# Performance work log

Measured on AMD Instinct MI355X. Metric: run time of the kernel, lower is better.

Reference implementation:

```python
import jax, jax.numpy as jnp
import numpy as np

L_SEQ = 32768
H_FEAT = 512
P_STATE = 256  # state_size // 2 (conj_sym)
LOG_DT_MIN, LOG_DT_MAX = np.log(1e-3), np.log(1e-1)


def setup_inputs() -> dict:
    key = jax.random.key(0)
    ks = jax.random.split(key, 7)
    input_sequence = jax.random.normal(ks[0], (L_SEQ, H_FEAT), dtype=jnp.float32)
    # eigenvalue real parts must be negative for stability (HiPPO-LegS-like)
    lambda_real = -jax.random.uniform(ks[1], (P_STATE,), minval=0.1, maxval=1.0, dtype=jnp.float32)
    lambda_imag = jax.random.normal(ks[2], (P_STATE,), dtype=jnp.float32) * float(np.pi)
    b = jax.random.normal(ks[3], (P_STATE, H_FEAT, 2), dtype=jnp.float32) / np.sqrt(H_FEAT)
    c = jax.random.normal(ks[4], (H_FEAT, P_STATE, 2), dtype=jnp.float32) / np.sqrt(P_STATE)
    d = jax.random.normal(ks[5], (H_FEAT,), dtype=jnp.float32)
    # log-timestep init in [log(1e-3), log(1e-1)] as in init_log_steps
    delta = (LOG_DT_MIN + jax.random.uniform(ks[6], (P_STATE, 1), dtype=jnp.float32)
             * (LOG_DT_MAX - LOG_DT_MIN))
    return {"input_sequence": input_sequence, "lambda_real": lambda_real,
            "lambda_imag": lambda_imag, "b": b, "c": c, "d": d, "delta": delta}


def _binop(e_i, e_j):
    A_i, b_i = e_i
    A_j, b_j = e_j
    return A_j * A_i, A_j * b_i + b_j


def reference(input_sequence, lambda_real, lambda_imag, b, c, d, delta):
    # assemble complex parameters (stored as real [..., 2])
    Lam = lambda_real + 1j * lambda_imag            # [P]
    B = b[..., 0] + 1j * b[..., 1]                  # [P, H]
    C = c[..., 0] + 1j * c[..., 1]                  # [H, P]
    step = jnp.exp(delta[:, 0])                     # step_rescale = 1.0
    # bilinear discretization
    BL = 1.0 / (1.0 - (step / 2.0) * Lam)
    Lam_bar = BL * (1.0 + (step / 2.0) * Lam)       # [P]
    B_bar = (BL * step)[:, None] * B                # [P, H]
    # input projection: Bu[l] = B_bar @ u[l]
    Bu = jnp.einsum('lh,ph->lp', input_sequence.astype(Lam_bar.dtype), B_bar)  # [L, P]
    L = input_sequence.shape[0]
    Lam_el = jnp.broadcast_to(Lam_bar, (L, Lam_bar.shape[0]))
    _, xs = jax.lax.associative_scan(_binop, (Lam_el, Bu))  # xs: [L, P] complex states
    # output projection (conj_sym => factor 2, real part)
    ys = 2.0 * jnp.einsum('lp,hp->lh', xs, C).real  # [L, H]
    return ys + d * input_sequence
```

## Files before the change

### kernel.cpp

```cpp
#include <hip/hip_runtime.h>
#include <cstddef>

#define L_SEQ 32768
#define H_FEAT 512
#define P_STATE 256
#define N2 512
#define CS 32
#define NCH (L_SEQ / CS)

typedef __bf16 bf16x8 __attribute__((ext_vector_type(8)));
typedef float f32x4 __attribute__((ext_vector_type(4)));

#define GLDS16(g, l) __builtin_amdgcn_global_load_lds( \
    (const __attribute__((address_space(1))) void*)(g), \
    (__attribute__((address_space(3))) void*)(l), 16, 0, 0)

__device__ __forceinline__ unsigned bf_rne(float x) {
    unsigned u = __float_as_uint(x);
    return (u + 0x7fffu + ((u >> 16) & 1u)) >> 16;
}
__device__ __forceinline__ float bf_f(unsigned bits) {
    return __uint_as_float(bits << 16);
}

__global__ __launch_bounds__(256) void param_kernel(
    const float* __restrict__ lr, const float* __restrict__ li,
    const float* __restrict__ b,  const float* __restrict__ c,
    const float* __restrict__ delta,
    ushort* __restrict__ W_hi, ushort* __restrict__ W_lo,
    ushort* __restrict__ C2_hi, ushort* __restrict__ C2_lo,
    float2* __restrict__ Abar)
{
    int tid = blockIdx.x * blockDim.x + threadIdx.x;

    {
        int p = tid >> 9;
        int h = tid & 511;
        float step = expf(delta[p]);
        float zr = 0.5f * step * lr[p];
        float zi = 0.5f * step * li[p];
        float dr = 1.0f - zr, di = -zi;
        float den = dr * dr + di * di;
        float blr = dr / den, bli = -di / den;
        float bbr = blr * step, bbi = bli * step;
        float b0 = b[((size_t)(p * H_FEAT + h)) * 2 + 0];
        float b1 = b[((size_t)(p * H_FEAT + h)) * 2 + 1];
        float vr = bbr * b0 - bbi * b1;
        float vi = bbr * b1 + bbi * b0;
        unsigned hr = bf_rne(vr), hl = bf_rne(vr - bf_f(hr));
        unsigned ir = bf_rne(vi), il = bf_rne(vi - bf_f(ir));
        size_t o0 = (size_t)(2 * p) * H_FEAT + h;
        size_t o1 = (size_t)(2 * p + 1) * H_FEAT + h;
        W_hi[o0] = (ushort)hr; W_lo[o0] = (ushort)hl;
        W_hi[o1] = (ushort)ir; W_lo[o1] = (ushort)il;
    }

    {
        int h2 = tid >> 8;
        int p2 = tid & 255;
        float c0 =  2.0f * c[((size_t)(h2 * P_STATE + p2)) * 2 + 0];
        float c1 = -2.0f * c[((size_t)(h2 * P_STATE + p2)) * 2 + 1];
        unsigned h0 = bf_rne(c0), l0 = bf_rne(c0 - bf_f(h0));
        unsigned h1 = bf_rne(c1), l1 = bf_rne(c1 - bf_f(h1));
        size_t o0 = (size_t)h2 * N2 + 2 * p2;
        C2_hi[o0] = (ushort)h0;     C2_lo[o0] = (ushort)l0;
        C2_hi[o0 + 1] = (ushort)h1; C2_lo[o0 + 1] = (ushort)l1;
    }

    if (tid < P_STATE) {
        int p = tid;
        float step = expf(delta[p]);
        float zr = 0.5f * step * lr[p];
        float zi = 0.5f * step * li[p];
        float dr = 1.0f - zr, di = -zi;
        float den = dr * dr + di * di;
        float blr = dr / den, bli = -di / den;
        float nr = 1.0f + zr, ni = zi;
        Abar[p] = make_float2(blr * nr - bli * ni, blr * ni + bli * nr);
    }
}

__global__ __launch_bounds__(256, 2) void gemm1(
    const float* __restrict__ A,
    const ushort* __restrict__ Bhi, const ushort* __restrict__ Blo,
    float* __restrict__ C)
{
    __shared__ ushort As_hi[128 * 32], As_lo[128 * 32];
    __shared__ ushort Bs_hi[256 * 32], Bs_lo[256 * 32];
    const int tid = threadIdx.x;
    const int ln = tid & 63, wv = tid >> 6;
    const int bm = blockIdx.y * 128, bn = blockIdx.x * 256;
    const int m = ln & 15, q = ln >> 4;
    const int wr = (wv >> 1) * 64, wc = (wv & 1) * 128;

    f32x4 acc[4][8] = {};

    for (int k0 = 0; k0 < 512; k0 += 32) {
#pragma unroll
        for (int s = 0; s < 8; s++) {
            int t = wv * 8 + s;
            int ch = t & 15;
            int row = ch * 16 + (ln >> 2);
            const ushort* src = (t < 16 ? Bhi : Blo)
                                + (size_t)(bn + row) * 512 + k0 + (ln & 3) * 8;
            ushort* dst = (t < 16 ? Bs_hi : Bs_lo) + ch * 512 + ln * 8;
            GLDS16(src, dst);
        }
#pragma unroll
        for (int r = 0; r < 4; r++) {
            int idx = tid + r * 256;
            int row = idx >> 3;
            int c4 = (idx & 7) << 2;
            const float4 v = *(const float4*)(A + (size_t)(bm + row) * 512 + k0 + c4);
            unsigned u0 = __float_as_uint(v.x), u1 = __float_as_uint(v.y);
            unsigned u2 = __float_as_uint(v.z), u3 = __float_as_uint(v.w);
            unsigned hi01 = (u0 >> 16) | (u1 & 0xffff0000u);
            unsigned hi23 = (u2 >> 16) | (u3 & 0xffff0000u);
            float d0 = v.x - __uint_as_float(u0 & 0xffff0000u);
            float d1 = v.y - __uint_as_float(u1 & 0xffff0000u);
            float d2 = v.z - __uint_as_float(u2 & 0xffff0000u);
            float d3 = v.w - __uint_as_float(u3 & 0xffff0000u);
            unsigned lo01 = (__float_as_uint(d0) >> 16) | (__float_as_uint(d1) & 0xffff0000u);
            unsigned lo23 = (__float_as_uint(d2) >> 16) | (__float_as_uint(d3) & 0xffff0000u);
            *(uint2*)(As_hi + row * 32 + c4) = make_uint2(hi01, hi23);
            *(uint2*)(As_lo + row * 32 + c4) = make_uint2(lo01, lo23);
        }
        __syncthreads();

        bf16x8 ah[4], al[4];
#pragma unroll
        for (int i = 0; i < 4; i++) {
            ah[i] = *(const bf16x8*)(As_hi + (wr + i * 16 + m) * 32 + q * 8);
            al[i] = *(const bf16x8*)(As_lo + (wr + i * 16 + m) * 32 + q * 8);
        }
#pragma unroll
        for (int j = 0; j < 8; j++) {
            bf16x8 bh = *(const bf16x8*)(Bs_hi + (wc + j * 16 + m) * 32 + q * 8);
            bf16x8 bl = *(const bf16x8*)(Bs_lo + (wc + j * 16 + m) * 32 + q * 8);
#pragma unroll
            for (int i = 0; i < 4; i++)
                acc[i][j] = __builtin_amdgcn_mfma_f32_16x16x32_bf16(ah[i], bh, acc[i][j], 0, 0, 0);
#pragma unroll
            for (int i = 0; i < 4; i++)
                acc[i][j] = __builtin_amdgcn_mfma_f32_16x16x32_bf16(al[i], bh, acc[i][j], 0, 0, 0);
#pragma unroll
            for (int i = 0; i < 4; i++)
                acc[i][j] = __builtin_amdgcn_mfma_f32_16x16x32_bf16(ah[i], bl, acc[i][j], 0, 0, 0);
        }
        __syncthreads();
    }

#pragma unroll
    for (int i = 0; i < 4; i++)
#pragma unroll
        for (int j = 0; j < 8; j++)
#pragma unroll
            for (int r = 0; r < 4; r++) {
                int row = bm + wr + i * 16 + q * 4 + r;
                int col = bn + wc + j * 16 + m;
                C[(size_t)row * 512 + col] = acc[i][j][r];
            }
}

__global__ __launch_bounds__(256, 2) void gemm2(
    const unsigned* __restrict__ Xp,
    const ushort* __restrict__ Bhi, const ushort* __restrict__ Blo,
    float* __restrict__ Cout, const float* __restrict__ U,
    const float* __restrict__ dvec)
{
    __shared__ ushort As_hi[128 * 32], As_lo[128 * 32];
    __shared__ ushort Bs_hi[256 * 32], Bs_lo[256 * 32];
    const int tid = threadIdx.x;
    const int ln = tid & 63, wv = tid >> 6;
    const int bm = blockIdx.y * 128, bn = blockIdx.x * 256;
    const int m = ln & 15, q = ln >> 4;
    const int wr = (wv >> 1) * 64, wc = (wv & 1) * 128;

    f32x4 acc[4][8] = {};

    for (int k0 = 0; k0 < 512; k0 += 32) {
#pragma unroll
        for (int s = 0; s < 8; s++) {
            int t = wv * 8 + s;
            int ch = t & 15;
            int row = ch * 16 + (ln >> 2);
            const ushort* src = (t < 16 ? Bhi : Blo)
                                + (size_t)(bn + row) * 512 + k0 + (ln & 3) * 8;
            ushort* dst = (t < 16 ? Bs_hi : Bs_lo) + ch * 512 + ln * 8;
            GLDS16(src, dst);
        }
#pragma unroll
        for (int r = 0; r < 4; r++) {
            int idx = tid + r * 256;
            int row = idx >> 3;
            int c4 = (idx & 7) << 2;
            const uint4 v = *(const uint4*)(Xp + (size_t)(bm + row) * 512 + k0 + c4);
            unsigned hi01 = (v.x >> 16) | (v.y & 0xffff0000u);
            unsigned hi23 = (v.z >> 16) | (v.w & 0xffff0000u);
            unsigned lo01 = (v.x & 0xffffu) | (v.y << 16);
            unsigned lo23 = (v.z & 0xffffu) | (v.w << 16);
            *(uint2*)(As_hi + row * 32 + c4) = make_uint2(hi01, hi23);
            *(uint2*)(As_lo + row * 32 + c4) = make_uint2(lo01, lo23);
        }
        __syncthreads();

        bf16x8 ah[4], al[4];
#pragma unroll
        for (int i = 0; i < 4; i++) {
            ah[i] = *(const bf16x8*)(As_hi + (wr + i * 16 + m) * 32 + q * 8);
            al[i] = *(const bf16x8*)(As_lo + (wr + i * 16 + m) * 32 + q * 8);
        }
#pragma unroll
        for (int j = 0; j < 8; j++) {
            bf16x8 bh = *(const bf16x8*)(Bs_hi + (wc + j * 16 + m) * 32 + q * 8);
            bf16x8 bl = *(const bf16x8*)(Bs_lo + (wc + j * 16 + m) * 32 + q * 8);
#pragma unroll
            for (int i = 0; i < 4; i++)
                acc[i][j] = __builtin_amdgcn_mfma_f32_16x16x32_bf16(ah[i], bh, acc[i][j], 0, 0, 0);
#pragma unroll
            for (int i = 0; i < 4; i++)
                acc[i][j] = __builtin_amdgcn_mfma_f32_16x16x32_bf16(al[i], bh, acc[i][j], 0, 0, 0);
#pragma unroll
            for (int i = 0; i < 4; i++)
                acc[i][j] = __builtin_amdgcn_mfma_f32_16x16x32_bf16(ah[i], bl, acc[i][j], 0, 0, 0);
        }
        __syncthreads();
    }

#pragma unroll
    for (int i = 0; i < 4; i++)
#pragma unroll
        for (int j = 0; j < 8; j++) {
            int col = bn + wc + j * 16 + m;
            float dv = dvec[col];
#pragma unroll
            for (int r = 0; r < 4; r++) {
                int row = bm + wr + i * 16 + q * 4 + r;
                Cout[(size_t)row * 512 + col] =
                    acc[i][j][r] + dv * U[(size_t)row * 512 + col];
            }
        }
}

__global__ __launch_bounds__(256) void scan_pass1(
    const float2* __restrict__ Bu, const float2* __restrict__ Abar,
    float2* __restrict__ ends)
{
    int tid = blockIdx.x * blockDim.x + threadIdx.x;
    int chunk = tid >> 8;
    int p = tid & 255;
    float2 A = Abar[p];
    float2 s = make_float2(0.f, 0.f);
    size_t base = (size_t)chunk * CS;
#pragma unroll 8
    for (int i = 0; i < CS; i++) {
        float2 u = Bu[(base + i) * P_STATE + p];
        float sr = fmaf(A.x, s.x, fmaf(-A.y, s.y, u.x));
        float si = fmaf(A.x, s.y, fmaf(A.y, s.x, u.y));
        s = make_float2(sr, si);
    }
    ends[(size_t)p * NCH + chunk] = s;
}

__global__ __launch_bounds__(1024) void scan_pass2(
    const float2* __restrict__ ends, const float2* __restrict__ Abar,
    float2* __restrict__ carries)
{
    __shared__ float2 sA[NCH];
    __shared__ float2 sB[NCH];
    int p = blockIdx.x;
    int t = threadIdx.x;

    float2 a = Abar[p];
#pragma unroll
    for (int i = 0; i < 5; i++) {
        float nr = a.x * a.x - a.y * a.y;
        float ni = 2.f * a.x * a.y;
        a = make_float2(nr, ni);
    }
    float2 A = a;
    float2 bv = ends[(size_t)p * NCH + t];
    sA[t] = A; sB[t] = bv;
    __syncthreads();

    for (int off = 1; off < NCH; off <<= 1) {
        float2 pa, pb;
        bool act = (t >= off);
        if (act) { pa = sA[t - off]; pb = sB[t - off]; }
        __syncthreads();
        if (act) {
            float2 nA = make_float2(A.x * pa.x - A.y * pa.y,
                                    A.x * pa.y + A.y * pa.x);
            float2 nB = make_float2(fmaf(A.x, pb.x, fmaf(-A.y, pb.y, bv.x)),
                                    fmaf(A.x, pb.y, fmaf(A.y, pb.x, bv.y)));
            A = nA; bv = nB;
            sA[t] = A; sB[t] = bv;
        }
        __syncthreads();
    }

    float2 carry = (t == 0) ? make_float2(0.f, 0.f) : sB[t - 1];
    carries[(size_t)p * NCH + t] = carry;
}

__global__ __launch_bounds__(256) void scan_pass3(
    uint2* __restrict__ Xp, const float2* __restrict__ Abar,
    const float2* __restrict__ carries)
{
    int tid = blockIdx.x * blockDim.x + threadIdx.x;
    int chunk = tid >> 8;
    int p = tid & 255;
    float2 A = Abar[p];
    float2 s = carries[(size_t)p * NCH + chunk];
    size_t base = (size_t)chunk * CS;
#pragma unroll 8
    for (int i = 0; i < CS; i++) {
        size_t off = (base + i) * P_STATE + p;
        uint2 ub = Xp[off];
        float ux = __uint_as_float(ub.x);
        float uy = __uint_as_float(ub.y);
        float sr = fmaf(A.x, s.x, fmaf(-A.y, s.y, ux));
        float si = fmaf(A.x, s.y, fmaf(A.y, s.x, uy));
        s = make_float2(sr, si);
        unsigned hr = bf_rne(sr);
        unsigned lr2 = __float_as_uint(sr - bf_f(hr)) >> 16;
        unsigned hi_ = bf_rne(si);
        unsigned li2 = __float_as_uint(si - bf_f(hi_)) >> 16;
        Xp[off] = make_uint2((hr << 16) | lr2, (hi_ << 16) | li2);
    }
}

extern "C" void kernel_launch(void* const* d_in, const int* in_sizes, int n_in,
                              void* d_out, int out_size, void* d_ws, size_t ws_size,
                              hipStream_t stream) {
    const float* u     = (const float*)d_in[0];
    const float* lr    = (const float*)d_in[1];
    const float* li    = (const float*)d_in[2];
    const float* b     = (const float*)d_in[3];
    const float* c     = (const float*)d_in[4];
    const float* dvec  = (const float*)d_in[5];
    const float* delta = (const float*)d_in[6];
    float* out = (float*)d_out;

    char* p = (char*)d_ws;
    float*  Bu      = (float*)p;   p += (size_t)L_SEQ * N2 * 4;
    float2* ends    = (float2*)p;  p += (size_t)P_STATE * NCH * 8;
    float2* carries = (float2*)p;  p += (size_t)P_STATE * NCH * 8;
    ushort* W_hi    = (ushort*)p;  p += (size_t)N2 * H_FEAT * 2;
    ushort* W_lo    = (ushort*)p;  p += (size_t)N2 * H_FEAT * 2;
    ushort* C2_hi   = (ushort*)p;  p += (size_t)H_FEAT * N2 * 2;
    ushort* C2_lo   = (ushort*)p;  p += (size_t)H_FEAT * N2 * 2;
    float2* Abar    = (float2*)p;  p += (size_t)P_STATE * 8;

    param_kernel<<<(P_STATE * H_FEAT) / 256, 256, 0, stream>>>(
        lr, li, b, c, delta, W_hi, W_lo, C2_hi, C2_lo, Abar);

    {
        dim3 grid(N2 / 256, L_SEQ / 128);
        gemm1<<<grid, 256, 0, stream>>>(u, W_hi, W_lo, Bu);
    }

    scan_pass1<<<(P_STATE * NCH) / 256, 256, 0, stream>>>(
        (const float2*)Bu, Abar, ends);
    scan_pass2<<<P_STATE, NCH, 0, stream>>>(ends, Abar, carries);
    scan_pass3<<<(P_STATE * NCH) / 256, 256, 0, stream>>>(
        (uint2*)Bu, Abar, carries);

    {
        dim3 grid(H_FEAT / 256, L_SEQ / 128);
        gemm2<<<grid, 256, 0, stream>>>((const unsigned*)Bu, C2_hi, C2_lo,
                                        out, u, dvec);
    }
}
```

Before: 254.0 us.

## Double-buffer B tiles and prefetch A into registers in both GEMMs

Both GEMM kernels now stage the next K-slice of B into a second LDS buffer via global_load_lds and load the next A slice into registers while MFMAs run on the current slice. The A split into bf16 hi/lo is written to LDS after the compute, between two barriers. This aims to hide global memory latency behind matrix math. In exchange it raises LDS use (B buffers doubled to about 80KB per block, which may limit the two-blocks-per-CU occupancy), adds register pressure and an extra barrier per iteration.

Result: slower. 267.0 us (+5.1%).

```diff
diff --git a/kernel.cpp b/kernel.cpp
--- a/kernel.cpp
+++ b/kernel.cpp
@@ -86,7 +86,7 @@
     float* __restrict__ C)
 {
     __shared__ ushort As_hi[128 * 32], As_lo[128 * 32];
-    __shared__ ushort Bs_hi[256 * 32], Bs_lo[256 * 32];
+    __shared__ ushort Bs_hi[2][256 * 32], Bs_lo[2][256 * 32];
     const int tid = threadIdx.x;
     const int ln = tid & 63, wv = tid >> 6;
     const int bm = blockIdx.y * 128, bn = blockIdx.x * 256;
@@ -95,7 +95,7 @@
 
     f32x4 acc[4][8] = {};
 
-    for (int k0 = 0; k0 < 512; k0 += 32) {
+    auto stageB = [&](int k0, int buf) {
 #pragma unroll
         for (int s = 0; s < 8; s++) {
             int t = wv * 8 + s;
@@ -103,15 +103,26 @@
             int row = ch * 16 + (ln >> 2);
             const ushort* src = (t < 16 ? Bhi : Blo)
                                 + (size_t)(bn + row) * 512 + k0 + (ln & 3) * 8;
-            ushort* dst = (t < 16 ? Bs_hi : Bs_lo) + ch * 512 + ln * 8;
+            ushort* dst = (t < 16 ? Bs_hi[buf] : Bs_lo[buf]) + ch * 512 + ln * 8;
             GLDS16(src, dst);
         }
+    };
+    auto loadA = [&](int k0, float4* av) {
 #pragma unroll
         for (int r = 0; r < 4; r++) {
             int idx = tid + r * 256;
             int row = idx >> 3;
             int c4 = (idx & 7) << 2;
-            const float4 v = *(const float4*)(A + (size_t)(bm + row) * 512 + k0 + c4);
+            av[r] = *(const float4*)(A + (size_t)(bm + row) * 512 + k0 + c4);
+        }
+    };
+    auto writeA = [&](const float4* av) {
+#pragma unroll
+        for (int r = 0; r < 4; r++) {
+            int idx = tid + r * 256;
+            int row = idx >> 3;
+            int c4 = (idx & 7) << 2;
+            const float4 v = av[r];
             unsigned u0 = __float_as_uint(v.x), u1 = __float_as_uint(v.y);
             unsigned u2 = __float_as_uint(v.z), u3 = __float_as_uint(v.w);
             unsigned hi01 = (u0 >> 16) | (u1 & 0xffff0000u);
@@ -125,7 +136,22 @@
             *(uint2*)(As_hi + row * 32 + c4) = make_uint2(hi01, hi23);
             *(uint2*)(As_lo + row * 32 + c4) = make_uint2(lo01, lo23);
         }
-        __syncthreads();
+    };
+
+    float4 av[4];
+    stageB(0, 0);
+    loadA(0, av);
+    writeA(av);
+    __syncthreads();
+
+    int cur = 0;
+    for (int t = 0; t < 16; t++) {
+        const int nk = t * 32 + 32;
+        const bool pf = (nk < 512);
+        if (pf) {
+            stageB(nk, cur ^ 1);
+            loadA(nk, av);
+        }
 
         bf16x8 ah[4], al[4];
 #pragma unroll
@@ -135,8 +161,8 @@
         }
 #pragma unroll
         for (int j = 0; j < 8; j++) {
-            bf16x8 bh = *(const bf16x8*)(Bs_hi + (wc + j * 16 + m) * 32 + q * 8);
-            bf16x8 bl = *(const bf16x8*)(Bs_lo + (wc + j * 16 + m) * 32 + q * 8);
+            bf16x8 bh = *(const bf16x8*)(Bs_hi[cur] + (wc + j * 16 + m) * 32 + q * 8);
+            bf16x8 bl = *(const bf16x8*)(Bs_lo[cur] + (wc + j * 16 + m) * 32 + q * 8);
 #pragma unroll
             for (int i = 0; i < 4; i++)
                 acc[i][j] = __builtin_amdgcn_mfma_f32_16x16x32_bf16(ah[i], bh, acc[i][j], 0, 0, 0);
@@ -148,6 +174,9 @@
                 acc[i][j] = __builtin_amdgcn_mfma_f32_16x16x32_bf16(ah[i], bl, acc[i][j], 0, 0, 0);
         }
         __syncthreads();
+        if (pf) writeA(av);
+        __syncthreads();
+        cur ^= 1;
     }
 
 #pragma unroll
@@ -169,7 +198,7 @@
     const float* __restrict__ dvec)
 {
     __shared__ ushort As_hi[128 * 32], As_lo[128 * 32];
-    __shared__ ushort Bs_hi[256 * 32], Bs_lo[256 * 32];
+    __shared__ ushort Bs_hi[2][256 * 32], Bs_lo[2][256 * 32];
     const int tid = threadIdx.x;
     const int ln = tid & 63, wv = tid >> 6;
     const int bm = blockIdx.y * 128, bn = blockIdx.x * 256;
@@ -178,7 +207,7 @@
 
     f32x4 acc[4][8] = {};
 
-    for (int k0 = 0; k0 < 512; k0 += 32) {
+    auto stageB = [&](int k0, int buf) {
 #pragma unroll
         for (int s = 0; s < 8; s++) {
             int t = wv * 8 + s;
@@ -186,15 +215,26 @@
             int row = ch * 16 + (ln >> 2);
             const ushort* src = (t < 16 ? Bhi : Blo)
                                 + (size_t)(bn + row) * 512 + k0 + (ln & 3) * 8;
-            ushort* dst = (t < 16 ? Bs_hi : Bs_lo) + ch * 512 + ln * 8;
+            ushort* dst = (t < 16 ? Bs_hi[buf] : Bs_lo[buf]) + ch * 512 + ln * 8;
             GLDS16(src, dst);
         }
+    };
+    auto loadA = [&](int k0, uint4* av) {
 #pragma unroll
         for (int r = 0; r < 4; r++) {
             int idx = tid + r * 256;
             int row = idx >> 3;
             int c4 = (idx & 7) << 2;
-            const uint4 v = *(const uint4*)(Xp + (size_t)(bm + row) * 512 + k0 + c4);
+            av[r] = *(const uint4*)(Xp + (size_t)(bm + row) * 512 + k0 + c4);
+        }
+    };
+    auto writeA = [&](const uint4* av) {
+#pragma unroll
+        for (int r = 0; r < 4; r++) {
+            int idx = tid + r * 256;
+            int row = idx >> 3;
+            int c4 = (idx & 7) << 2;
+            const uint4 v = av[r];
             unsigned hi01 = (v.x >> 16) | (v.y & 0xffff0000u);
             unsigned hi23 = (v.z >> 16) | (v.w & 0xffff0000u);
             unsigned lo01 = (v.x & 0xffffu) | (v.y << 16);
@@ -202,7 +242,22 @@
             *(uint2*)(As_hi + row * 32 + c4) = make_uint2(hi01, hi23);
             *(uint2*)(As_lo + row * 32 + c4) = make_uint2(lo01, lo23);
         }
-        __syncthreads();
+    };
+
+    uint4 av[4];
+    stageB(0, 0);
+    loadA(0, av);
+    writeA(av);
+    __syncthreads();
+
+    int cur = 0;
+    for (int t = 0; t < 16; t++) {
+        const int nk = t * 32 + 32;
+        const bool pf = (nk < 512);
+        if (pf) {
+            stageB(nk, cur ^ 1);
+            loadA(nk, av);
+        }
 
         bf16x8 ah[4], al[4];
 #pragma unroll
@@ -212,8 +267,8 @@
         }
 #pragma unroll
         for (int j = 0; j < 8; j++) {
-            bf16x8 bh = *(const bf16x8*)(Bs_hi + (wc + j * 16 + m) * 32 + q * 8);
-            bf16x8 bl = *(const bf16x8*)(Bs_lo + (wc + j * 16 + m) * 32 + q * 8);
+            bf16x8 bh = *(const bf16x8*)(Bs_hi[cur] + (wc + j * 16 + m) * 32 + q * 8);
+            bf16x8 bl = *(const bf16x8*)(Bs_lo[cur] + (wc + j * 16 + m) * 32 + q * 8);
 #pragma unroll
             for (int i = 0; i < 4; i++)
                 acc[i][j] = __builtin_amdgcn_mfma_f32_16x16x32_bf16(ah[i], bh, acc[i][j], 0, 0, 0);
@@ -225,6 +280,9 @@
                 acc[i][j] = __builtin_amdgcn_mfma_f32_16x16x32_bf16(ah[i], bl, acc[i][j], 0, 0, 0);
         }
         __syncthreads();
+        if (pf) writeA(av);
+        __syncthreads();
+        cur ^= 1;
     }
 
 #pragma unroll
```

## Double-buffer B tiles and load A fragments directly to registers in GEMMs

Applied to the files above, without the earlier changes.

Both GEMM kernels now keep two LDS buffers for the B operand so the next k-slice is prefetched with global_load_lds while the current one is computed. The A operand skips LDS entirely: each lane loads its MFMA fragment straight from global memory and splits it into hi/lo bf16 in registers. Manual vmcnt waits, raw s_barrier calls and sched_barrier fences replace __syncthreads. This removes an LDS round trip and one barrier per iteration, at the cost of less coalesced A loads, more register pressure, and fragile hand-tuned wait counts.

New measurement: 282.5 us. +11.2%, slower.

```diff
diff --git a/kernel.cpp b/kernel.cpp
--- a/kernel.cpp
+++ b/kernel.cpp
@@ -14,6 +14,8 @@
 #define GLDS16(g, l) __builtin_amdgcn_global_load_lds( \
     (const __attribute__((address_space(1))) void*)(g), \
     (__attribute__((address_space(3))) void*)(l), 16, 0, 0)
+
+#define SCHED_FENCE() __builtin_amdgcn_sched_barrier(0)
 
 __device__ __forceinline__ unsigned bf_rne(float x) {
     unsigned u = __float_as_uint(x);
@@ -85,8 +87,7 @@
     const ushort* __restrict__ Bhi, const ushort* __restrict__ Blo,
     float* __restrict__ C)
 {
-    __shared__ ushort As_hi[128 * 32], As_lo[128 * 32];
-    __shared__ ushort Bs_hi[256 * 32], Bs_lo[256 * 32];
+    __shared__ ushort Bs_hi[2][256 * 32], Bs_lo[2][256 * 32];
     const int tid = threadIdx.x;
     const int ln = tid & 63, wv = tid >> 6;
     const int bm = blockIdx.y * 128, bn = blockIdx.x * 256;
@@ -95,7 +96,7 @@
 
     f32x4 acc[4][8] = {};
 
-    for (int k0 = 0; k0 < 512; k0 += 32) {
+    auto stageB = [&](int k0, int buf) {
 #pragma unroll
         for (int s = 0; s < 8; s++) {
             int t = wv * 8 + s;
@@ -103,40 +104,55 @@
             int row = ch * 16 + (ln >> 2);
             const ushort* src = (t < 16 ? Bhi : Blo)
                                 + (size_t)(bn + row) * 512 + k0 + (ln & 3) * 8;
-            ushort* dst = (t < 16 ? Bs_hi : Bs_lo) + ch * 512 + ln * 8;
+            ushort* dst = (t < 16 ? Bs_hi[buf] : Bs_lo[buf]) + ch * 512 + ln * 8;
             GLDS16(src, dst);
         }
-#pragma unroll
-        for (int r = 0; r < 4; r++) {
-            int idx = tid + r * 256;
-            int row = idx >> 3;
-            int c4 = (idx & 7) << 2;
-            const float4 v = *(const float4*)(A + (size_t)(bm + row) * 512 + k0 + c4);
-            unsigned u0 = __float_as_uint(v.x), u1 = __float_as_uint(v.y);
-            unsigned u2 = __float_as_uint(v.z), u3 = __float_as_uint(v.w);
-            unsigned hi01 = (u0 >> 16) | (u1 & 0xffff0000u);
-            unsigned hi23 = (u2 >> 16) | (u3 & 0xffff0000u);
-            float d0 = v.x - __uint_as_float(u0 & 0xffff0000u);
-            float d1 = v.y - __uint_as_float(u1 & 0xffff0000u);
-            float d2 = v.z - __uint_as_float(u2 & 0xffff0000u);
-            float d3 = v.w - __uint_as_float(u3 & 0xffff0000u);
-            unsigned lo01 = (__float_as_uint(d0) >> 16) | (__float_as_uint(d1) & 0xffff0000u);
-            unsigned lo23 = (__float_as_uint(d2) >> 16) | (__float_as_uint(d3) & 0xffff0000u);
-            *(uint2*)(As_hi + row * 32 + c4) = make_uint2(hi01, hi23);
-            *(uint2*)(As_lo + row * 32 + c4) = make_uint2(lo01, lo23);
-        }
-        __syncthreads();
-
-        bf16x8 ah[4], al[4];
+    };
+
+    const float* a0 = A + (size_t)(bm + wr + m) * 512 + q * 8;
+
+    auto loadAfrag = [&](int k0, f32x4* av0, f32x4* av1) {
 #pragma unroll
         for (int i = 0; i < 4; i++) {
-            ah[i] = *(const bf16x8*)(As_hi + (wr + i * 16 + m) * 32 + q * 8);
-            al[i] = *(const bf16x8*)(As_lo + (wr + i * 16 + m) * 32 + q * 8);
-        }
+            const float* src = a0 + (size_t)i * 16 * 512 + k0;
+            av0[i] = *(const f32x4*)src;
+            av1[i] = *(const f32x4*)(src + 4);
+        }
+    };
+    auto cvtA = [&](const f32x4* av0, const f32x4* av1, bf16x8* ah, bf16x8* al) {
+#pragma unroll
+        for (int i = 0; i < 4; i++) {
+            unsigned b0 = __float_as_uint(av0[i][0]), b1 = __float_as_uint(av0[i][1]);
+            unsigned b2 = __float_as_uint(av0[i][2]), b3 = __float_as_uint(av0[i][3]);
+            unsigned b4 = __float_as_uint(av1[i][0]), b5 = __float_as_uint(av1[i][1]);
+            unsigned b6 = __float_as_uint(av1[i][2]), b7 = __float_as_uint(av1[i][3]);
+            uint4 hw = make_uint4((b0 >> 16) | (b1 & 0xffff0000u),
+                                  (b2 >> 16) | (b3 & 0xffff0000u),
+                                  (b4 >> 16) | (b5 & 0xffff0000u),
+                                  (b6 >> 16) | (b7 & 0xffff0000u));
+            float d0 = av0[i][0] - __uint_as_float(b0 & 0xffff0000u);
+            float d1 = av0[i][1] - __uint_as_float(b1 & 0xffff0000u);
+            float d2 = av0[i][2] - __uint_as_float(b2 & 0xffff0000u);
+            float d3 = av0[i][3] - __uint_as_float(b3 & 0xffff0000u);
+            float d4 = av1[i][0] - __uint_as_float(b4 & 0xffff0000u);
+            float d5 = av1[i][1] - __uint_as_float(b5 & 0xffff0000u);
+            float d6 = av1[i][2] - __uint_as_float(b6 & 0xffff0000u);
+            float d7 = av1[i][3] - __uint_as_float(b7 & 0xffff0000u);
+            uint4 lw = make_uint4((__float_as_uint(d0) >> 16) | (__float_as_uint(d1) & 0xffff0000u),
+                                  (__float_as_uint(d2) >> 16) | (__float_as_uint(d3) & 0xffff0000u),
+                                  (__float_as_uint(d4) >> 16) | (__float_as_uint(d5) & 0xffff0000u),
+                                  (__float_as_uint(d6) >> 16) | (__float_as_uint(d7) & 0xffff0000u));
+            ah[i] = *(bf16x8*)&hw;
+            al[i] = *(bf16x8*)&lw;
+        }
+    };
+    auto compute = [&](int buf, const bf16x8* ah, const bf16x8* al) {
+        const ushort* bsh = Bs_hi[buf];
+        const ushort* bsl = Bs_lo[buf];
 #pragma unroll
         for (int j = 0; j < 8; j++) {
-            bf16x8 bh = *(const bf16x8*)(Bs_hi + (wc + j * 16 + m) * 32 + q * 8);
-            bf16x8 bl = *(const bf16x8*)(Bs_lo + (wc + j * 16 + m) * 32 + q * 8);
+            bf16x8 bh = *(const bf16x8*)(bsh + (wc + j * 16 + m) * 32 + q * 8);
+            bf16x8 bl = *(const bf16x8*)(bsl + (wc + j * 16 + m) * 32 + q * 8);
 #pragma unroll
             for (int i = 0; i < 4; i++)
                 acc[i][j] = __builtin_amdgcn_mfma_f32_16x16x32_bf16(ah[i], bh, acc[i][j], 0, 0, 0);
@@ -147,8 +163,32 @@
             for (int i = 0; i < 4; i++)
                 acc[i][j] = __builtin_amdgcn_mfma_f32_16x16x32_bf16(ah[i], bl, acc[i][j], 0, 0, 0);
         }
-        __syncthreads();
-    }
+    };
+
+    stageB(0, 0);
+
+    f32x4 av0[4], av1[4];
+    bf16x8 ah[4], al[4];
+
+    for (int t = 0; t < 15; t++) {
+        const int k0 = t * 32;
+        loadAfrag(k0, av0, av1);
+        SCHED_FENCE();
+        stageB(k0 + 32, (t + 1) & 1);
+        SCHED_FENCE();
+        cvtA(av0, av1, ah, al);
+        asm volatile("s_waitcnt vmcnt(8)" ::: "memory");
+        SCHED_FENCE();
+        __builtin_amdgcn_s_barrier();
+        compute(t & 1, ah, al);
+        __builtin_amdgcn_s_barrier();
+    }
+    loadAfrag(480, av0, av1);
+    cvtA(av0, av1, ah, al);
+    asm volatile("s_waitcnt vmcnt(0)" ::: "memory");
+    SCHED_FENCE();
+    __builtin_amdgcn_s_barrier();
+    compute(1, ah, al);
 
 #pragma unroll
     for (int i = 0; i < 4; i++)
@@ -168,8 +208,7 @@
     float* __restrict__ Cout, const float* __restrict__ U,
     const float* __restrict__ dvec)
 {
-    __shared__ ushort As_hi[128 * 32], As_lo[128 * 32];
-    __shared__ ushort Bs_hi[256 * 32], Bs_lo[256 * 32];
+    __shared__ ushort Bs_hi[2][256 * 32], Bs_lo[2][256 * 32];
     const int tid = threadIdx.x;
     const int ln = tid & 63, wv = tid >> 6;
     const int bm = blockIdx.y * 128, bn = blockIdx.x * 256;
@@ -178,7 +217,7 @@
 
     f32x4 acc[4][8] = {};
 
-    for (int k0 = 0; k0 < 512; k0 += 32) {
+    auto stageB = [&](int k0, int buf) {
 #pragma unroll
         for (int s = 0; s < 8; s++) {
             int t = wv * 8 + s;
@@ -186,34 +225,43 @@
             int row = ch * 16 + (ln >> 2);
             const ushort* src = (t < 16 ? Bhi : Blo)
                                 + (size_t)(bn + row) * 512 + k0 + (ln & 3) * 8;
-            ushort* dst = (t < 16 ? Bs_hi : Bs_lo) + ch * 512 + ln * 8;
+            ushort* dst = (t < 16 ? Bs_hi[buf] : Bs_lo[buf]) + ch * 512 + ln * 8;
             GLDS16(src, dst);
         }
-#pragma unroll
-        for (int r = 0; r < 4; r++) {
-            int idx = tid + r * 256;
-            int row = idx >> 3;
-            int c4 = (idx & 7) << 2;
-            const uint4 v = *(const uint4*)(Xp + (size_t)(bm + row) * 512 + k0 + c4);
-            unsigned hi01 = (v.x >> 16) | (v.y & 0xffff0000u);
-            unsigned hi23 = (v.z >> 16) | (v.w & 0xffff0000u);
-            unsigned lo01 = (v.x & 0xffffu) | (v.y << 16);
-            unsigned lo23 = (v.z & 0xffffu) | (v.w << 16);
-            *(uint2*)(As_hi + row * 32 + c4) = make_uint2(hi01, hi23);
-            *(uint2*)(As_lo + row * 32 + c4) = make_uint2(lo01, lo23);
-        }
-        __syncthreads();
-
-        bf16x8 ah[4], al[4];
+    };
+
+    const unsigned* x0 = Xp + (size_t)(bm + wr + m) * 512 + q * 8;
+
+    auto loadAfrag = [&](int k0, uint4* av0, uint4* av1) {
 #pragma unroll
         for (int i = 0; i < 4; i++) {
-            ah[i] = *(const bf16x8*)(As_hi + (wr + i * 16 + m) * 32 + q * 8);
-            al[i] = *(const bf16x8*)(As_lo + (wr + i * 16 + m) * 32 + q * 8);
-        }
+            const unsigned* src = x0 + (size_t)i * 16 * 512 + k0;
+            av0[i] = *(const uint4*)src;
+            av1[i] = *(const uint4*)(src + 4);
+        }
+    };
+    auto cvtA = [&](const uint4* av0, const uint4* av1, bf16x8* ah, bf16x8* al) {
+#pragma unroll
+        for (int i = 0; i < 4; i++) {
+            uint4 hw = make_uint4((av0[i].x >> 16) | (av0[i].y & 0xffff0000u),
+                                  (av0[i].z >> 16) | (av0[i].w & 0xffff0000u),
+                                  (av1[i].x >> 16) | (av1[i].y & 0xffff0000u),
+                                  (av1[i].z >> 16) | (av1[i].w & 0xffff0000u));
+            uint4 lw = make_uint4((av0[i].x & 0xffffu) | (av0[i].y << 16),
+                                  (av0[i].z & 0xffffu) | (av0[i].w << 16),
+                                  (av1[i].x & 0xffffu) | (av1[i].y << 16),
+                                  (av1[i].z & 0xffffu) | (av1[i].w << 16));
+            ah[i] = *(bf16x8*)&hw;
+            al[i] = *(bf16x8*)&lw;
+        }
+    };
+    auto compute = [&](int buf, const bf16x8* ah, const bf16x8* al) {
+        const ushort* bsh = Bs_hi[buf];
+        const ushort* bsl = Bs_lo[buf];
 #pragma unroll
         for (int j = 0; j < 8; j++) {
-            bf16x8 bh = *(const bf16x8*)(Bs_hi + (wc + j * 16 + m) * 32 + q * 8);
-            bf16x8 bl = *(const bf16x8*)(Bs_lo + (wc + j * 16 + m) * 32 + q * 8);
+            bf16x8 bh = *(const bf16x8*)(bsh + (wc + j * 16 + m) * 32 + q * 8);
+            bf16x8 bl = *(const bf16x8*)(bsl + (wc + j * 16 + m) * 32 + q * 8);
 #pragma unroll
             for (int i = 0; i < 4; i++)
                 acc[i][j] = __builtin_amdgcn_mfma_f32_16x16x32_bf16(ah[i], bh, acc[i][j], 0, 0, 0);
@@ -224,8 +272,32 @@
             for (int i = 0; i < 4; i++)
                 acc[i][j] = __builtin_amdgcn_mfma_f32_16x16x32_bf16(ah[i], bl, acc[i][j], 0, 0, 0);
         }
-        __syncthreads();
-    }
+    };
+
+    stageB(0, 0);
+
+    uint4 av0[4], av1[4];
+    bf16x8 ah[4], al[4];
+
+    for (int t = 0; t < 15; t++) {
+        const int k0 = t * 32;
+        loadAfrag(k0, av0, av1);
+        SCHED_FENCE();
+        stageB(k0 + 32, (t + 1) & 1);
+        SCHED_FENCE();
+        cvtA(av0, av1, ah, al);
+        asm volatile("s_waitcnt vmcnt(8)" ::: "memory");
+        SCHED_FENCE();
+        __builtin_amdgcn_s_barrier();
+        compute(t & 1, ah, al);
+        __builtin_amdgcn_s_barrier();
+    }
+    loadAfrag(480, av0, av1);
+    cvtA(av0, av1, ah, al);
+    asm volatile("s_waitcnt vmcnt(0)" ::: "memory");
+    SCHED_FENCE();
+    __builtin_amdgcn_s_barrier();
+    compute(1, ah, al);
 
 #pragma unroll
     for (int i = 0; i < 4; i++)
```

## Fuse chunk scan passes into GEMM epilogue and GEMM2 prologue

Applied to the files above, without the earlier changes.

Folds the per-chunk partial scan (pass 1) into gemm1's epilogue, staging accumulator tiles through shared memory to compute chunk end states. It also folds the carry-applied rescan (pass 3) into gemm2's A-tile loading, where it performs the bf16 hi/lo split on the fly. This removes two kernel launches and two full read/write sweeps of the Bu buffer. In exchange the scan in both GEMMs runs serially on only 128 or 64 threads while the other threads wait at barriers, and gemm2 needs extra shared memory, which may reduce occupancy.

Result: faster. 246.3 us (-3.0%).

```diff
diff --git a/kernel.cpp b/kernel.cpp
--- a/kernel.cpp
+++ b/kernel.cpp
@@ -83,10 +83,16 @@
 __global__ __launch_bounds__(256, 2) void gemm1(
     const float* __restrict__ A,
     const ushort* __restrict__ Bhi, const ushort* __restrict__ Blo,
-    float* __restrict__ C)
+    float* __restrict__ C,
+    const float2* __restrict__ Abar, float2* __restrict__ ends)
 {
-    __shared__ ushort As_hi[128 * 32], As_lo[128 * 32];
-    __shared__ ushort Bs_hi[256 * 32], Bs_lo[256 * 32];
+    __shared__ ushort sh[24576];
+    ushort* As_hi = sh;
+    ushort* As_lo = sh + 4096;
+    ushort* Bs_hi = sh + 8192;
+    ushort* Bs_lo = sh + 16384;
+    float*  Cs    = (float*)(sh + 8192);
+
     const int tid = threadIdx.x;
     const int ln = tid & 63, wv = tid >> 6;
     const int bm = blockIdx.y * 128, bn = blockIdx.x * 256;
@@ -160,16 +166,48 @@
                 int col = bn + wc + j * 16 + m;
                 C[(size_t)row * 512 + col] = acc[i][j][r];
             }
+
+    float2 Aop;
+    if (tid < 128) Aop = Abar[(bn >> 1) + tid];
+#pragma unroll
+    for (int c = 0; c < 4; c++) {
+        if ((wv >> 1) == (c >> 1)) {
+#pragma unroll
+            for (int ii = 0; ii < 2; ii++) {
+                int i = (c & 1) * 2 + ii;
+#pragma unroll
+                for (int j = 0; j < 8; j++)
+#pragma unroll
+                    for (int r = 0; r < 4; r++)
+                        Cs[(ii * 16 + q * 4 + r) * 256 + wc + j * 16 + m] = acc[i][j][r];
+            }
+        }
+        __syncthreads();
+        if (tid < 128) {
+            float2 s = make_float2(0.f, 0.f);
+#pragma unroll 8
+            for (int i2 = 0; i2 < 32; i2++) {
+                float2 u = *(const float2*)(Cs + i2 * 256 + 2 * tid);
+                float sr = fmaf(Aop.x, s.x, fmaf(-Aop.y, s.y, u.x));
+                float si = fmaf(Aop.x, s.y, fmaf(Aop.y, s.x, u.y));
+                s = make_float2(sr, si);
+            }
+            ends[(size_t)((bn >> 1) + tid) * NCH + (bm >> 5) + c] = s;
+        }
+        __syncthreads();
+    }
 }
 
 __global__ __launch_bounds__(256, 2) void gemm2(
-    const unsigned* __restrict__ Xp,
+    const float* __restrict__ Bu,
     const ushort* __restrict__ Bhi, const ushort* __restrict__ Blo,
     float* __restrict__ Cout, const float* __restrict__ U,
-    const float* __restrict__ dvec)
+    const float* __restrict__ dvec,
+    const float2* __restrict__ Abar, const float2* __restrict__ carries)
 {
     __shared__ ushort As_hi[128 * 32], As_lo[128 * 32];
     __shared__ ushort Bs_hi[256 * 32], Bs_lo[256 * 32];
+    __shared__ float  Af32[128 * 32];
     const int tid = threadIdx.x;
     const int ln = tid & 63, wv = tid >> 6;
     const int bm = blockIdx.y * 128, bn = blockIdx.x * 256;
@@ -194,13 +232,30 @@
             int idx = tid + r * 256;
             int row = idx >> 3;
             int c4 = (idx & 7) << 2;
-            const uint4 v = *(const uint4*)(Xp + (size_t)(bm + row) * 512 + k0 + c4);
-            unsigned hi01 = (v.x >> 16) | (v.y & 0xffff0000u);
-            unsigned hi23 = (v.z >> 16) | (v.w & 0xffff0000u);
-            unsigned lo01 = (v.x & 0xffffu) | (v.y << 16);
-            unsigned lo23 = (v.z & 0xffffu) | (v.w << 16);
-            *(uint2*)(As_hi + row * 32 + c4) = make_uint2(hi01, hi23);
-            *(uint2*)(As_lo + row * 32 + c4) = make_uint2(lo01, lo23);
+            const float4 v = *(const float4*)(Bu + (size_t)(bm + row) * 512 + k0 + c4);
+            *(float4*)(Af32 + row * 32 + c4) = v;
+        }
+        __syncthreads();
+
+        if (tid < 64) {
+            const int pl = tid & 15, ch = tid >> 4;
+            const int pg = (k0 >> 1) + pl;
+            const float2 Aop = Abar[pg];
+            float2 s = carries[(size_t)pg * NCH + (bm >> 5) + ch];
+#pragma unroll 8
+            for (int i = 0; i < 32; i++) {
+                const int row = ch * 32 + i;
+                const float2 uv = *(const float2*)(Af32 + row * 32 + 2 * pl);
+                float sr = fmaf(Aop.x, s.x, fmaf(-Aop.y, s.y, uv.x));
+                float si = fmaf(Aop.x, s.y, fmaf(Aop.y, s.x, uv.y));
+                s = make_float2(sr, si);
+                unsigned hr  = bf_rne(sr);
+                unsigned lr2 = __float_as_uint(sr - bf_f(hr)) >> 16;
+                unsigned hi_ = bf_rne(si);
+                unsigned li2 = __float_as_uint(si - bf_f(hi_)) >> 16;
+                *(unsigned*)(As_hi + row * 32 + 2 * pl) = hr | (hi_ << 16);
+                *(unsigned*)(As_lo + row * 32 + 2 * pl) = lr2 | (li2 << 16);
+            }
         }
         __syncthreads();
 
@@ -240,26 +295,6 @@
                     acc[i][j][r] + dv * U[(size_t)row * 512 + col];
             }
         }
-}
-
-__global__ __launch_bounds__(256) void scan_pass1(
-    const float2* __restrict__ Bu, const float2* __restrict__ Abar,
-    float2* __restrict__ ends)
-{
-    int tid = blockIdx.x * blockDim.x + threadIdx.x;
-    int chunk = tid >> 8;
-    int p = tid & 255;
-    float2 A = Abar[p];
-    float2 s = make_float2(0.f, 0.f);
-    size_t base = (size_t)chunk * CS;
-#pragma unroll 8
-    for (int i = 0; i < CS; i++) {
-        float2 u = Bu[(base + i) * P_STATE + p];
-        float sr = fmaf(A.x, s.x, fmaf(-A.y, s.y, u.x));
-        float si = fmaf(A.x, s.y, fmaf(A.y, s.x, u.y));
-        s = make_float2(sr, si);
-    }
-    ends[(size_t)p * NCH + chunk] = s;
 }
 
 __global__ __launch_bounds__(1024) void scan_pass2(
@@ -301,33 +336,6 @@
 
     float2 carry = (t == 0) ? make_float2(0.f, 0.f) : sB[t - 1];
     carries[(size_t)p * NCH + t] = carry;
-}
-
-__global__ __launch_bounds__(256) void scan_pass3(
-    uint2* __restrict__ Xp, const float2* __restrict__ Abar,
-    const float2* __restrict__ carries)
-{
-    int tid = blockIdx.x * blockDim.x + threadIdx.x;
-    int chunk = tid >> 8;
-    int p = tid & 255;
-    float2 A = Abar[p];
-    float2 s = carries[(size_t)p * NCH + chunk];
-    size_t base = (size_t)chunk * CS;
-#pragma unroll 8
-    for (int i = 0; i < CS; i++) {
-        size_t off = (base + i) * P_STATE + p;
-        uint2 ub = Xp[off];
-        float ux = __uint_as_float(ub.x);
-        float uy = __uint_as_float(ub.y);
-        float sr = fmaf(A.x, s.x, fmaf(-A.y, s.y, ux));
-        float si = fmaf(A.x, s.y, fmaf(A.y, s.x, uy));
-        s = make_float2(sr, si);
-        unsigned hr = bf_rne(sr);
-        unsigned lr2 = __float_as_uint(sr - bf_f(hr)) >> 16;
-        unsigned hi_ = bf_rne(si);
-        unsigned li2 = __float_as_uint(si - bf_f(hi_)) >> 16;
-        Xp[off] = make_uint2((hr << 16) | lr2, (hi_ << 16) | li2);
-    }
 }
 
 extern "C" void kernel_launch(void* const* d_in, const int* in_sizes, int n_in,
@@ -357,18 +365,14 @@
 
     {
         dim3 grid(N2 / 256, L_SEQ / 128);
-        gemm1<<<grid, 256, 0, stream>>>(u, W_hi, W_lo, Bu);
-    }
-
-    scan_pass1<<<(P_STATE * NCH) / 256, 256, 0, stream>>>(
-        (const float2*)Bu, Abar, ends);
+        gemm1<<<grid, 256, 0, stream>>>(u, W_hi, W_lo, Bu, Abar, ends);
+    }
+
     scan_pass2<<<P_STATE, NCH, 0, stream>>>(ends, Abar, carries);
-    scan_pass3<<<(P_STATE * NCH) / 256, 256, 0, stream>>>(
-        (uint2*)Bu, Abar, carries);
 
     {
         dim3 grid(H_FEAT / 256, L_SEQ / 128);
-        gemm2<<<grid, 256, 0, stream>>>((const unsigned*)Bu, C2_hi, C2_lo,
-                                        out, u, dvec);
-    }
-}
+        gemm2<<<grid, 256, 0, stream>>>(Bu, C2_hi, C2_lo, out, u, dvec,
+                                        Abar, carries);
+    }
+}
```
